# Performance work log

Measured on AMD Instinct MI355X. Metric: run time of the kernel, lower is better.

The kernel has to match this reference:

```python
import jax, jax.numpy as jnp
import numpy as np

H = 12          # trees_num / n_heads
D_WEIGHT = 0.1  # opt['d_weight']
NEG = -1e9


def setup_inputs() -> dict:
    key = jax.random.key(0)
    ks = jax.random.split(key, 6)
    B, N, D = 8, 512, 768
    inp = {}
    inp["input"] = jax.random.normal(ks[0], (B, N, D), dtype=jnp.float32)
    inp["src_mask"] = jax.random.randint(ks[1], (B, 1, N), 0, 2).astype(jnp.int32)
    inp["dep_emb"] = jax.random.normal(ks[2], (B, N, N), dtype=jnp.float32)
    s = 1.0 / np.sqrt(D)
    inp["Wq"] = jax.random.normal(ks[3], (D, D), dtype=jnp.float32) * s
    inp["bq"] = jnp.zeros((D,), dtype=jnp.float32)
    inp["Wk"] = jax.random.normal(ks[4], (D, D), dtype=jnp.float32) * s
    inp["bk"] = jnp.zeros((D,), dtype=jnp.float32)
    return inp


def reference(input, src_mask, dep_emb, Wq, bq, Wk, bk):
    B, N, D = input.shape
    dk = D // H
    # Q/K projections -> [B, H, N, dk]
    q = (input @ Wq + bq).reshape(B, N, H, dk).transpose(0, 2, 1, 3)
    k = (input @ Wk + bk).reshape(B, N, H, dk).transpose(0, 2, 1, 3)
    # scaled scores [B, H, N, N]
    scores = jnp.einsum("bhqd,bhkd->bhqk", q, k) / jnp.sqrt(jnp.asarray(dk, input.dtype))
    # blend with dependency bias: dep_emb [B,N,N] -> [B,1,N,N]
    scores = (1.0 - D_WEIGHT) * scores + D_WEIGHT * dep_emb[:, None, :, :]
    # mask: src_mask [B,1,N] -> [B,1,1,N]; masked_fill(mask==0, -1e9)
    scores = jnp.where(src_mask[:, None, :, :] == 0, NEG, scores)
    p_attn = jax.nn.softmax(scores, axis=-1)  # [B, H, N, N]
    # original returns list of per-head [B,N,N]; full tensor is equivalent
    return p_attn
```

## Files before the change

kernel.cpp:

```cpp
#include <hip/hip_runtime.h>


typedef _Float16 f16;
typedef _Float16 f16x4 __attribute__((ext_vector_type(4)));
typedef _Float16 f16x8 __attribute__((ext_vector_type(8)));
typedef float    f32x4 __attribute__((ext_vector_type(4)));

#define NTOK   512
#define DMODEL 768
#define BATCH  8
#define NHEAD  12
#define NEGV   (-1e9f)
#define KPAD   72
#define DEPS   516
#define OUTS   68

__global__ __launch_bounds__(256)
void prep_kernel(const float* __restrict__ X, f16* __restrict__ Xh,
                 const float* __restrict__ Wq, const float* __restrict__ Wk,
                 f16* __restrict__ Wt) {
    const int bx = blockIdx.x;
    if (bx < 3072) {
        const size_t i = ((size_t)bx * 256 + threadIdx.x) * 4;
        float4 v = *(const float4*)&X[i];
        f16x4 h = { (f16)v.x, (f16)v.y, (f16)v.z, (f16)v.w };
        *(f16x4*)&Xh[i] = h;
    } else {
        __shared__ float tile[32][33];
        const int id = bx - 3072;
        const int kb = (id % 24) * 32;
        const int nb = (id / 24) * 32;
        const float* __restrict__ W = (nb < 768) ? Wq : Wk;
        const int nc = (nb < 768) ? nb : nb - 768;
        const int tx = threadIdx.x & 31, ty = threadIdx.x >> 5;
        #pragma unroll
        for (int i = 0; i < 4; ++i)
            tile[ty + i*8][tx] = W[(size_t)(kb + ty + i*8) * DMODEL + nc + tx];
        __syncthreads();
        #pragma unroll
        for (int i = 0; i < 4; ++i)
            Wt[(size_t)(nb + ty + i*8) * DMODEL + kb + tx] = (f16)tile[tx][ty + i*8];
    }
}

__global__ __launch_bounds__(256)
void proj_mfma(const f16* __restrict__ Xh, const f16* __restrict__ Wt,
               const float* __restrict__ bq, const float* __restrict__ bk,
               f16* __restrict__ QK) {
    const int m0 = blockIdx.x * 128;
    const int n0 = blockIdx.y * 128;
    const int tid = threadIdx.x;
    const int wid = tid >> 6, l = tid & 63;
    const int l15 = l & 15, quad = l >> 4;
    const int wm = (wid & 1) * 64;
    const int wn = (wid >> 1) * 64;

    __shared__ f16 As[128 * KPAD];
    __shared__ f16 Bs[128 * KPAD];

    f32x4 acc[4][4];
    #pragma unroll
    for (int i = 0; i < 4; ++i)
        #pragma unroll
        for (int j = 0; j < 4; ++j) acc[i][j] = (f32x4){0.f, 0.f, 0.f, 0.f};

    const int srow = tid >> 1;
    const int scol = (tid & 1) * 32;

    for (int kt = 0; kt < DMODEL; kt += 64) {
        const f16* __restrict__ Asrc = Xh + (size_t)(m0 + srow) * DMODEL + kt + scol;
        const f16* __restrict__ Bsrc = Wt + (size_t)(n0 + srow) * DMODEL + kt + scol;
        #pragma unroll
        for (int j = 0; j < 4; ++j) {
            f16x8 av = *(const f16x8*)(Asrc + j * 8);
            *(f16x8*)&As[srow * KPAD + scol + j * 8] = av;
        }
        #pragma unroll
        for (int j = 0; j < 4; ++j) {
            f16x8 bv = *(const f16x8*)(Bsrc + j * 8);
            *(f16x8*)&Bs[srow * KPAD + scol + j * 8] = bv;
        }
        __syncthreads();
        #pragma unroll
        for (int ks = 0; ks < 2; ++ks) {
            f16x8 a[4], b[4];
            #pragma unroll
            for (int mi = 0; mi < 4; ++mi)
                a[mi] = *(f16x8*)&As[(wm + mi*16 + l15) * KPAD + ks*32 + quad*8];
            #pragma unroll
            for (int ni = 0; ni < 4; ++ni)
                b[ni] = *(f16x8*)&Bs[(wn + ni*16 + l15) * KPAD + ks*32 + quad*8];
            #pragma unroll
            for (int mi = 0; mi < 4; ++mi)
                #pragma unroll
                for (int ni = 0; ni < 4; ++ni)
                    acc[mi][ni] = __builtin_amdgcn_mfma_f32_16x16x32_f16(
                        a[mi], b[ni], acc[mi][ni], 0, 0, 0);
        }
        __syncthreads();
    }

    const float SC = (1.0f - 0.1f) / 8.0f;
    #pragma unroll
    for (int ni = 0; ni < 4; ++ni) {
        const int col = n0 + wn + ni * 16 + l15;
        const bool isQ = (col < 768);
        const float bv = isQ ? bq[col] : bk[col - 768];
        const float sc = isQ ? SC : 1.0f;
        #pragma unroll
        for (int mi = 0; mi < 4; ++mi)
            #pragma unroll
            for (int r = 0; r < 4; ++r) {
                const int row = m0 + wm + mi * 16 + quad * 4 + r;
                QK[(size_t)row * 1536 + col] = (f16)((acc[mi][ni][r] + bv) * sc);
            }
    }
}

__global__ __launch_bounds__(384, 2)
void attn_mfma(const f16* __restrict__ QK, const float* __restrict__ dep,
               const int* __restrict__ mask, float* __restrict__ out) {
    const int qt = blockIdx.x;
    const int hg = blockIdx.y;
    const int b  = blockIdx.z;
    const int tid = threadIdx.x;
    const int wid = tid >> 6;
    const int l   = tid & 63;
    const int l15 = l & 15, quad = l >> 4;
    const int h  = hg * 6 + wid;
    const int q0 = qt * 16;

    __shared__ float depL[16 * DEPS];
    __shared__ float outL[6 * 16 * OUTS];

    {
        const float* __restrict__ src = dep + ((size_t)b * NTOK + q0) * NTOK;
        #pragma unroll
        for (int i = 0; i < 6; ++i) {
            const int idx = tid + i * 384;
            if (idx < 2048) {
                const int row = idx >> 7, c4 = idx & 127;
                float4 v = *(const float4*)&src[(size_t)row * NTOK + c4 * 4];
                *(float4*)&depL[row * DEPS + c4 * 4] = v;
            }
        }
    }
    __syncthreads();

    f32x4 acc[32];
    #pragma unroll
    for (int t = 0; t < 32; ++t) acc[t] = (f32x4){0.f, 0.f, 0.f, 0.f};

    const f16* __restrict__ Qb = QK + (size_t)(b * NTOK + q0 + l15) * 1536 + h * 64 + quad * 8;
    const f16x8 qf0 = *(const f16x8*)(Qb);
    const f16x8 qf1 = *(const f16x8*)(Qb + 32);

    const f16* __restrict__ Kb = QK + (size_t)(b * NTOK + l15) * 1536 + 768 + h * 64 + quad * 8;
    #pragma unroll
    for (int t = 0; t < 32; ++t) {
        f16x8 k0 = *(const f16x8*)(Kb + (size_t)(t * 16) * 1536);
        acc[t] = __builtin_amdgcn_mfma_f32_16x16x32_f16(qf0, k0, acc[t], 0, 0, 0);
        f16x8 k1 = *(const f16x8*)(Kb + (size_t)(t * 16) * 1536 + 32);
        acc[t] = __builtin_amdgcn_mfma_f32_16x16x32_f16(qf1, k1, acc[t], 0, 0, 0);
    }

    const float DW = 0.1f;
    const int* __restrict__ mrow = mask + b * NTOK;
    #pragma unroll
    for (int t = 0; t < 32; ++t) {
        const int col = t * 16 + l15;
        const int mv = mrow[col];
        #pragma unroll
        for (int r = 0; r < 4; ++r) {
            const float dv = depL[(quad * 4 + r) * DEPS + col];
            const float s = acc[t][r] + DW * dv;
            acc[t][r] = mv ? s : NEGV;
        }
    }

    float rmax[4] = {NEGV, NEGV, NEGV, NEGV};
    #pragma unroll
    for (int t = 0; t < 32; ++t)
        #pragma unroll
        for (int r = 0; r < 4; ++r) rmax[r] = fmaxf(rmax[r], acc[t][r]);
    #pragma unroll
    for (int r = 0; r < 4; ++r) {
        rmax[r] = fmaxf(rmax[r], __shfl_xor(rmax[r], 1));
        rmax[r] = fmaxf(rmax[r], __shfl_xor(rmax[r], 2));
        rmax[r] = fmaxf(rmax[r], __shfl_xor(rmax[r], 4));
        rmax[r] = fmaxf(rmax[r], __shfl_xor(rmax[r], 8));
    }
    float rsum[4] = {0.f, 0.f, 0.f, 0.f};
    #pragma unroll
    for (int t = 0; t < 32; ++t)
        #pragma unroll
        for (int r = 0; r < 4; ++r) {
            const float e = __expf(acc[t][r] - rmax[r]);
            acc[t][r] = e;
            rsum[r] += e;
        }
    #pragma unroll
    for (int r = 0; r < 4; ++r) {
        rsum[r] += __shfl_xor(rsum[r], 1);
        rsum[r] += __shfl_xor(rsum[r], 2);
        rsum[r] += __shfl_xor(rsum[r], 4);
        rsum[r] += __shfl_xor(rsum[r], 8);
    }
    float inv[4];
    #pragma unroll
    for (int r = 0; r < 4; ++r) inv[r] = 1.0f / rsum[r];

    float* __restrict__ wOut = &outL[wid * 16 * OUTS];
    const size_t obase = ((size_t)((b * NHEAD + h) * NTOK) + q0) * NTOK;
    #pragma unroll
    for (int c = 0; c < 8; ++c) {
        #pragma unroll
        for (int tc = 0; tc < 4; ++tc) {
            const int t = c * 4 + tc;
            #pragma unroll
            for (int r = 0; r < 4; ++r)
                wOut[(quad * 4 + r) * OUTS + tc * 16 + l15] = acc[t][r] * inv[r];
        }
        #pragma unroll
        for (int j = 0; j < 4; ++j) {
            const int row = j * 4 + quad;
            const int c4  = l15;
            float4 v = *(float4*)&wOut[row * OUTS + c4 * 4];
            *(float4*)&out[obase + (size_t)row * NTOK + c * 64 + c4 * 4] = v;
        }
    }
}

extern "C" void kernel_launch(void* const* d_in, const int* in_sizes, int n_in,
                              void* d_out, int out_size, void* d_ws, size_t ws_size,
                              hipStream_t stream) {
    const float* X    = (const float*)d_in[0];
    const int*   mask = (const int*)  d_in[1];
    const float* dep  = (const float*)d_in[2];
    const float* Wq   = (const float*)d_in[3];
    const float* bq   = (const float*)d_in[4];
    const float* Wk   = (const float*)d_in[5];
    const float* bk   = (const float*)d_in[6];
    float* out = (float*)d_out;

    f16* Xh = (f16*)d_ws;
    f16* Wt = Xh + (size_t)BATCH * NTOK * DMODEL;
    f16* QK = Wt + (size_t)1536 * DMODEL;

    prep_kernel<<<dim3(3072 + 1152), 256, 0, stream>>>(X, Xh, Wq, Wk, Wt);
    proj_mfma<<<dim3(4096 / 128, 1536 / 128), 256, 0, stream>>>(Xh, Wt, bq, bk, QK);
    attn_mfma<<<dim3(32, 2, BATCH), 384, 0, stream>>>(QK, dep, mask, out);
}
```

Before: 185.4 us.

## Transpose MFMA operands so each lane owns a query row and stores directly

Swaps the A/B operands of the QK^T MFMA so the accumulator layout puts one query row per lane group with four consecutive key columns per register. Mask and dependency values are then read as vectors, and the softmax reductions use two cross-quad shuffles on a single scalar instead of four shuffles on four values. Each lane writes its results straight to global memory as float4, dropping the shared-memory output staging buffer. The barrier after the dep-tile load is moved after the MFMA loop so the global-to-LDS copy overlaps the matrix math. Each wave's stores now cover 16 rows with 16-byte chunks per lane, 64 contiguous bytes per row per store, which may coalesce less well than the previous staged row writes.

```diff
diff --git a/kernel.cpp b/kernel.cpp
--- a/kernel.cpp
+++ b/kernel.cpp
@@ -13,7 +13,6 @@
 #define NEGV   (-1e9f)
 #define KPAD   72
 #define DEPS   516
-#define OUTS   68
 
 __global__ __launch_bounds__(256)
 void prep_kernel(const float* __restrict__ X, f16* __restrict__ Xh,
@@ -131,7 +130,6 @@
     const int q0 = qt * 16;
 
     __shared__ float depL[16 * DEPS];
-    __shared__ float outL[6 * 16 * OUTS];
 
     {
         const float* __restrict__ src = dep + ((size_t)b * NTOK + q0) * NTOK;
@@ -145,7 +143,6 @@
             }
         }
     }
-    __syncthreads();
 
     f32x4 acc[32];
     #pragma unroll
@@ -159,75 +156,53 @@
     #pragma unroll
     for (int t = 0; t < 32; ++t) {
         f16x8 k0 = *(const f16x8*)(Kb + (size_t)(t * 16) * 1536);
-        acc[t] = __builtin_amdgcn_mfma_f32_16x16x32_f16(qf0, k0, acc[t], 0, 0, 0);
+        acc[t] = __builtin_amdgcn_mfma_f32_16x16x32_f16(k0, qf0, acc[t], 0, 0, 0);
         f16x8 k1 = *(const f16x8*)(Kb + (size_t)(t * 16) * 1536 + 32);
-        acc[t] = __builtin_amdgcn_mfma_f32_16x16x32_f16(qf1, k1, acc[t], 0, 0, 0);
-    }
+        acc[t] = __builtin_amdgcn_mfma_f32_16x16x32_f16(k1, qf1, acc[t], 0, 0, 0);
+    }
+
+    __syncthreads();
 
     const float DW = 0.1f;
     const int* __restrict__ mrow = mask + b * NTOK;
-    #pragma unroll
-    for (int t = 0; t < 32; ++t) {
-        const int col = t * 16 + l15;
-        const int mv = mrow[col];
+    float m = NEGV;
+    #pragma unroll
+    for (int t = 0; t < 32; ++t) {
+        const int kc = t * 16 + quad * 4;
+        const f32x4 dv = *(const f32x4*)&depL[l15 * DEPS + kc];
+        const int4  mv = *(const int4*)&mrow[kc];
+        const float s0 = acc[t][0] + DW * dv[0];
+        const float s1 = acc[t][1] + DW * dv[1];
+        const float s2 = acc[t][2] + DW * dv[2];
+        const float s3 = acc[t][3] + DW * dv[3];
+        acc[t][0] = mv.x ? s0 : NEGV;
+        acc[t][1] = mv.y ? s1 : NEGV;
+        acc[t][2] = mv.z ? s2 : NEGV;
+        acc[t][3] = mv.w ? s3 : NEGV;
+        m = fmaxf(m, fmaxf(fmaxf(acc[t][0], acc[t][1]), fmaxf(acc[t][2], acc[t][3])));
+    }
+    m = fmaxf(m, __shfl_xor(m, 16));
+    m = fmaxf(m, __shfl_xor(m, 32));
+
+    float sum = 0.f;
+    #pragma unroll
+    for (int t = 0; t < 32; ++t) {
         #pragma unroll
         for (int r = 0; r < 4; ++r) {
-            const float dv = depL[(quad * 4 + r) * DEPS + col];
-            const float s = acc[t][r] + DW * dv;
-            acc[t][r] = mv ? s : NEGV;
-        }
-    }
-
-    float rmax[4] = {NEGV, NEGV, NEGV, NEGV};
-    #pragma unroll
-    for (int t = 0; t < 32; ++t)
-        #pragma unroll
-        for (int r = 0; r < 4; ++r) rmax[r] = fmaxf(rmax[r], acc[t][r]);
-    #pragma unroll
-    for (int r = 0; r < 4; ++r) {
-        rmax[r] = fmaxf(rmax[r], __shfl_xor(rmax[r], 1));
-        rmax[r] = fmaxf(rmax[r], __shfl_xor(rmax[r], 2));
-        rmax[r] = fmaxf(rmax[r], __shfl_xor(rmax[r], 4));
-        rmax[r] = fmaxf(rmax[r], __shfl_xor(rmax[r], 8));
-    }
-    float rsum[4] = {0.f, 0.f, 0.f, 0.f};
-    #pragma unroll
-    for (int t = 0; t < 32; ++t)
-        #pragma unroll
-        for (int r = 0; r < 4; ++r) {
-            const float e = __expf(acc[t][r] - rmax[r]);
+            const float e = __expf(acc[t][r] - m);
             acc[t][r] = e;
-            rsum[r] += e;
-        }
-    #pragma unroll
-    for (int r = 0; r < 4; ++r) {
-        rsum[r] += __shfl_xor(rsum[r], 1);
-        rsum[r] += __shfl_xor(rsum[r], 2);
-        rsum[r] += __shfl_xor(rsum[r], 4);
-        rsum[r] += __shfl_xor(rsum[r], 8);
-    }
-    float inv[4];
-    #pragma unroll
-    for (int r = 0; r < 4; ++r) inv[r] = 1.0f / rsum[r];
-
-    float* __restrict__ wOut = &outL[wid * 16 * OUTS];
-    const size_t obase = ((size_t)((b * NHEAD + h) * NTOK) + q0) * NTOK;
-    #pragma unroll
-    for (int c = 0; c < 8; ++c) {
-        #pragma unroll
-        for (int tc = 0; tc < 4; ++tc) {
-            const int t = c * 4 + tc;
-            #pragma unroll
-            for (int r = 0; r < 4; ++r)
-                wOut[(quad * 4 + r) * OUTS + tc * 16 + l15] = acc[t][r] * inv[r];
-        }
-        #pragma unroll
-        for (int j = 0; j < 4; ++j) {
-            const int row = j * 4 + quad;
-            const int c4  = l15;
-            float4 v = *(float4*)&wOut[row * OUTS + c4 * 4];
-            *(float4*)&out[obase + (size_t)row * NTOK + c * 64 + c4 * 4] = v;
-        }
+            sum += e;
+        }
+    }
+    sum += __shfl_xor(sum, 16);
+    sum += __shfl_xor(sum, 32);
+    const float inv = 1.0f / sum;
+
+    const size_t obase = ((size_t)((b * NHEAD + h) * NTOK) + q0 + l15) * NTOK + quad * 4;
+    #pragma unroll
+    for (int t = 0; t < 32; ++t) {
+        f32x4 v = acc[t] * inv;
+        *(f32x4*)&out[obase + (size_t)t * 16] = v;
     }
 }
 
```

Result: slower. 189.8 us (median of 2 runs) (+2.3%).
